# Kernel tuning notes

Measured on AMD Instinct MI355X. Metric: run time of the kernel, lower is better.

## Reference

```python
import jax, jax.numpy as jnp
import numpy as np

B = 32
N_INPUTS = 16384
N_DET = 65536
K = 32  # max_inputs_per_detector


def setup_inputs() -> dict:
    key = jax.random.key(0)
    k1, k2 = jax.random.split(key)
    x = jax.random.normal(k1, (B, N_INPUTS), dtype=jnp.float32)
    # detector membership table: each detector watches K input neuron ids
    detectors = jax.random.randint(k2, (N_DET, K), 0, N_INPUTS, dtype=jnp.int32)
    return {"x": x, "detectors": detectors}


def reference(x, detectors):
    """Winner-take-all inhibition.

    For each batch row and each detector, the member input with the largest
    activation is the winner; every other (valid, id != -1) member is
    inhibited (its winning_stat is incremented). Output spikes (1.0) only for
    inputs never inhibited by any detector (winning_stat == 0), matching
    spiking_inhibition=True where the output is a pure binary mask.
    """
    Bn, n_inputs = x.shape
    D, Kd = detectors.shape
    valid = detectors >= 0                      # [D, K] (-1 = padding)
    safe_idx = jnp.where(valid, detectors, 0)   # [D, K]
    neg_inf = jnp.float32(-jnp.inf)
    col = jnp.arange(Kd, dtype=jnp.int32)[None, :]

    def per_batch(xb):  # xb: [n_inputs]
        vals = jnp.where(valid, xb[safe_idx], neg_inf)     # [D, K] gather
        widx = jnp.argmax(vals, axis=-1)                   # winner slot per detector
        loser = valid & (col != widx[:, None])             # inhibited members
        stat = jnp.zeros((n_inputs,), jnp.int32).at[safe_idx.reshape(-1)].add(
            loser.reshape(-1).astype(jnp.int32))           # scatter-add counts
        return stat

    stat = jax.vmap(per_batch)(x)               # [B, n_inputs]
    out = (stat == 0).astype(jnp.float32)       # spike iff never inhibited
    return out
```

## Files before the change

### kernel.cpp

```cpp
#include <hip/hip_runtime.h>

#define N_INPUTS 16384
#define N_DET    65536
#define KD       32
#define BATCH    32
#define SLICES   16
#define PAIRS    (BATCH / 2)
#define DPB      (N_DET / SLICES)
#define THREADS  1024

#define DEG_BLOCKS     64
#define DET_PER_DEGBLK (N_DET / DEG_BLOCKS)
#define DEG_WORDS      (N_INPUTS / 4)
#define WC_WORDS       (N_INPUTS / 2)

__device__ __forceinline__ float max3f(float a, float b, float c) {
    return fmaxf(fmaxf(a, b), c);
}


__global__ __launch_bounds__(1024) void degree_count(const int* __restrict__ det,
                                                     unsigned* __restrict__ degp) {
    __shared__ unsigned dl[DEG_WORDS];
    const int tid = threadIdx.x;
#pragma unroll
    for (int k = 0; k < DEG_WORDS / 1024; ++k) dl[tid + k * 1024] = 0u;
    __syncthreads();

    const int d = blockIdx.x * DET_PER_DEGBLK + tid;
    const int4* drow = (const int4*)det + (size_t)d * (KD / 4);
#pragma unroll
    for (int q = 0; q < KD / 4; ++q) {
        int4 r = drow[q];
        atomicAdd(&dl[r.x >> 2], 1u << (8 * (r.x & 3)));
        atomicAdd(&dl[r.y >> 2], 1u << (8 * (r.y & 3)));
        atomicAdd(&dl[r.z >> 2], 1u << (8 * (r.z & 3)));
        atomicAdd(&dl[r.w >> 2], 1u << (8 * (r.w & 3)));
    }
    __syncthreads();

    unsigned* out = degp + (size_t)blockIdx.x * DEG_WORDS;
#pragma unroll
    for (int k = 0; k < DEG_WORDS / 1024; ++k)
        out[tid + k * 1024] = dl[tid + k * 1024];
}

__global__ __launch_bounds__(THREADS) void inhibit(const float* __restrict__ x,
                                                   const int* __restrict__ det,
                                                   unsigned* __restrict__ wp) {
    __shared__ float2   xs[N_INPUTS];
    __shared__ unsigned wc[WC_WORDS];

    const int slice = blockIdx.x;
    const int pair  = blockIdx.y;
    const int tid   = threadIdx.x;

#pragma unroll
    for (int k = 0; k < WC_WORDS / THREADS; ++k) wc[tid + k * THREADS] = 0u;

    const float4* x0 = (const float4*)(x + (size_t)(2 * pair) * N_INPUTS);
    const float4* x1 = (const float4*)(x + (size_t)(2 * pair + 1) * N_INPUTS);
    float4* xs4 = (float4*)xs;
#pragma unroll
    for (int k = 0; k < N_INPUTS / 4 / THREADS; ++k) {
        int t = tid + k * THREADS;
        float4 a = x0[t], b = x1[t];
        xs4[2 * t + 0] = make_float4(a.x, b.x, a.y, b.y);
        xs4[2 * t + 1] = make_float4(a.z, b.z, a.w, b.w);
    }
    __syncthreads();

    const int4* det4 = (const int4*)det;
#pragma unroll 1
    for (int j = 0; j < DPB / THREADS; ++j) {
        const int   d    = slice * DPB + j * THREADS + tid;
        const int4* drow = det4 + (size_t)d * 8;
        int ids[KD];
#pragma unroll
        for (int q = 0; q < 8; ++q) {
            int4 r = drow[q];
            ids[q * 4 + 0] = r.x; ids[q * 4 + 1] = r.y;
            ids[q * 4 + 2] = r.z; ids[q * 4 + 3] = r.w;
        }

        float2 v[KD];
#pragma unroll
        for (int s = 0; s < KD; ++s) v[s] = xs[ids[s]];

        float t0[11], t1[11];
#pragma unroll
        for (int i = 0; i < 10; ++i) {
            t0[i] = max3f(v[3 * i].x, v[3 * i + 1].x, v[3 * i + 2].x);
            t1[i] = max3f(v[3 * i].y, v[3 * i + 1].y, v[3 * i + 2].y);
        }
        t0[10] = fmaxf(v[30].x, v[31].x);
        t1[10] = fmaxf(v[30].y, v[31].y);
        float m0 = fmaxf(max3f(max3f(t0[0], t0[1], t0[2]),
                               max3f(t0[3], t0[4], t0[5]),
                               max3f(t0[6], t0[7], t0[8])),
                         fmaxf(t0[9], t0[10]));
        float m1 = fmaxf(max3f(max3f(t1[0], t1[1], t1[2]),
                               max3f(t1[3], t1[4], t1[5]),
                               max3f(t1[6], t1[7], t1[8])),
                         fmaxf(t1[9], t1[10]));

        int i0 = ids[0], i1 = ids[0];
#pragma unroll
        for (int s = KD - 1; s >= 0; --s) {
            i0 = (v[s].x == m0) ? ids[s] : i0;
            i1 = (v[s].y == m1) ? ids[s] : i1;
        }

        atomicAdd(&wc[i0 >> 1], 1u << (8 * ((i0 & 1) * 2 + 0)));
        atomicAdd(&wc[i1 >> 1], 1u << (8 * ((i1 & 1) * 2 + 1)));
    }
    __syncthreads();

    unsigned* out = wp + (size_t)(slice * PAIRS + pair) * WC_WORDS;
#pragma unroll
    for (int k = 0; k < WC_WORDS / THREADS; ++k)
        out[tid + k * THREADS] = wc[tid + k * THREADS];
}

__global__ __launch_bounds__(1024) void finalize(const unsigned* __restrict__ wp,
                                                 const unsigned* __restrict__ degp,
                                                 float* __restrict__ out) {
    __shared__ unsigned red[1024];
    const int k = blockIdx.x, t = threadIdx.x;

    red[t] = degp[(size_t)(t >> 4) * DEG_WORDS + k * 16 + (t & 15)];
    __syncthreads();
#pragma unroll
    for (int off = 512; off >= 16; off >>= 1) {
        if (t < off) red[t] += red[t + off];
        __syncthreads();
    }

    const int b  = t & 31;
    const int jp = t >> 5;
    const int p  = b >> 1, q = b & 1;

    unsigned wsum = 0;
#pragma unroll
    for (int s = 0; s < SLICES; ++s)
        wsum += wp[(size_t)(s * PAIRS + p) * WC_WORDS + k * 32 + jp];

    const unsigned w0 = (wsum >> (8 * q)) & 255u;
    const unsigned w1 = (wsum >> (8 * (2 + q))) & 255u;

    const unsigned dw = red[jp >> 1];
    const int      sh = (2 * jp) & 3;
    const unsigned d0 = (dw >> (8 * sh)) & 255u;
    const unsigned d1 = (dw >> (8 * (sh + 1))) & 255u;

    float2 r;
    r.x = (w0 == d0) ? 1.0f : 0.0f;
    r.y = (w1 == d1) ? 1.0f : 0.0f;
    const size_t i0 = (size_t)k * 64 + 2 * jp;
    *(float2*)(out + (size_t)b * N_INPUTS + i0) = r;
}

extern "C" void kernel_launch(void* const* d_in, const int* in_sizes, int n_in,
                              void* d_out, int out_size, void* d_ws, size_t ws_size,
                              hipStream_t stream) {
    const float* x   = (const float*)d_in[0];
    const int*   det = (const int*)d_in[1];
    unsigned* wp   = (unsigned*)d_ws;
    unsigned* degp = (unsigned*)d_ws + (size_t)SLICES * PAIRS * WC_WORDS;

    degree_count<<<DEG_BLOCKS, 1024, 0, stream>>>(det, degp);
    dim3 grid(SLICES, PAIRS);
    inhibit<<<grid, THREADS, 0, stream>>>(x, det, wp);
    finalize<<<N_INPUTS / 64, 1024, 0, stream>>>(wp, degp, (float*)d_out);
}
```

Measured before the change: 98.80 us.

## Hoist degree reduction into separate kernel and flatten finalize to coalesced per-element writes

Adds a degree_reduce kernel that sums the 64 per-block packed degree partials once into a single array. Previously every finalize block did a shared-memory tree reduction over those partials. Finalize now runs one thread per output element with 256-thread blocks, giving fully coalesced scalar stores. It reads the pre-reduced degree word and sums the 16 slice partials of the winner counts. In exchange there is an extra kernel launch, and each winner-count word is now read by more threads, roughly doubling redundant wp loads that the cache must absorb.

New measurement: 94.13 us. 1.05x faster.

```diff
diff --git a/kernel.cpp b/kernel.cpp
--- a/kernel.cpp
+++ b/kernel.cpp
@@ -43,6 +43,15 @@
 #pragma unroll
     for (int k = 0; k < DEG_WORDS / 1024; ++k)
         out[tid + k * 1024] = dl[tid + k * 1024];
+}
+
+__global__ __launch_bounds__(256) void degree_reduce(const unsigned* __restrict__ degp,
+                                                     unsigned* __restrict__ degf) {
+    const int w = blockIdx.x * 256 + threadIdx.x;
+    unsigned s = 0;
+#pragma unroll
+    for (int p = 0; p < DEG_BLOCKS; ++p) s += degp[(size_t)p * DEG_WORDS + w];
+    degf[w] = s;
 }
 
 __global__ __launch_bounds__(THREADS) void inhibit(const float* __restrict__ x,
@@ -122,42 +131,22 @@
         out[tid + k * THREADS] = wc[tid + k * THREADS];
 }
 
-__global__ __launch_bounds__(1024) void finalize(const unsigned* __restrict__ wp,
-                                                 const unsigned* __restrict__ degp,
-                                                 float* __restrict__ out) {
-    __shared__ unsigned red[1024];
-    const int k = blockIdx.x, t = threadIdx.x;
-
-    red[t] = degp[(size_t)(t >> 4) * DEG_WORDS + k * 16 + (t & 15)];
-    __syncthreads();
-#pragma unroll
-    for (int off = 512; off >= 16; off >>= 1) {
-        if (t < off) red[t] += red[t + off];
-        __syncthreads();
-    }
-
-    const int b  = t & 31;
-    const int jp = t >> 5;
-    const int p  = b >> 1, q = b & 1;
+__global__ __launch_bounds__(256) void finalize(const unsigned* __restrict__ wp,
+                                                const unsigned* __restrict__ degf,
+                                                float* __restrict__ out) {
+    const int gid = blockIdx.x * 256 + threadIdx.x;
+    const int b   = gid >> 14;
+    const int i   = gid & (N_INPUTS - 1);
+    const int p   = b >> 1, q = b & 1;
 
     unsigned wsum = 0;
 #pragma unroll
     for (int s = 0; s < SLICES; ++s)
-        wsum += wp[(size_t)(s * PAIRS + p) * WC_WORDS + k * 32 + jp];
+        wsum += wp[(size_t)(s * PAIRS + p) * WC_WORDS + (i >> 1)];
 
-    const unsigned w0 = (wsum >> (8 * q)) & 255u;
-    const unsigned w1 = (wsum >> (8 * (2 + q))) & 255u;
-
-    const unsigned dw = red[jp >> 1];
-    const int      sh = (2 * jp) & 3;
-    const unsigned d0 = (dw >> (8 * sh)) & 255u;
-    const unsigned d1 = (dw >> (8 * (sh + 1))) & 255u;
-
-    float2 r;
-    r.x = (w0 == d0) ? 1.0f : 0.0f;
-    r.y = (w1 == d1) ? 1.0f : 0.0f;
-    const size_t i0 = (size_t)k * 64 + 2 * jp;
-    *(float2*)(out + (size_t)b * N_INPUTS + i0) = r;
+    const unsigned win = (wsum >> (8 * ((i & 1) * 2 + q))) & 255u;
+    const unsigned deg = (degf[i >> 2] >> (8 * (i & 3))) & 255u;
+    out[gid] = (win == deg) ? 1.0f : 0.0f;
 }
 
 extern "C" void kernel_launch(void* const* d_in, const int* in_sizes, int n_in,
@@ -166,10 +155,12 @@
     const float* x   = (const float*)d_in[0];
     const int*   det = (const int*)d_in[1];
     unsigned* wp   = (unsigned*)d_ws;
-    unsigned* degp = (unsigned*)d_ws + (size_t)SLICES * PAIRS * WC_WORDS;
+    unsigned* degp = wp + (size_t)SLICES * PAIRS * WC_WORDS;
+    unsigned* degf = degp + (size_t)DEG_BLOCKS * DEG_WORDS;
 
     degree_count<<<DEG_BLOCKS, 1024, 0, stream>>>(det, degp);
+    degree_reduce<<<DEG_WORDS / 256, 256, 0, stream>>>(degp, degf);
     dim3 grid(SLICES, PAIRS);
     inhibit<<<grid, THREADS, 0, stream>>>(x, det, wp);
-    finalize<<<N_INPUTS / 64, 1024, 0, stream>>>(wp, degp, (float*)d_out);
+    finalize<<<BATCH * N_INPUTS / 256, 256, 0, stream>>>(wp, degf, (float*)d_out);
 }
```
